# Kernel optimization log

Measured on AMD Instinct MI355X. Metric: run time of the kernel, lower is better.

## Reference

```python
import jax, jax.numpy as jnp
import numpy as np

D_MODEL = 1024
N_HEADS = 16
DEPTH = D_MODEL // N_HEADS
B, S = 2, 2048


def setup_inputs() -> dict:
    key = jax.random.key(0)
    ks = jax.random.split(key, 11)
    scale = 1.0 / np.sqrt(D_MODEL)
    return {
        "q": jax.random.normal(ks[0], (B, S, D_MODEL), jnp.float32),
        "k": jax.random.normal(ks[1], (B, S, D_MODEL), jnp.float32),
        "v": jax.random.normal(ks[2], (B, S, D_MODEL), jnp.float32),
        "wq": jax.random.normal(ks[3], (D_MODEL, D_MODEL), jnp.float32) * scale,
        "bq": jnp.zeros((D_MODEL,), jnp.float32),
        "wk": jax.random.normal(ks[4], (D_MODEL, D_MODEL), jnp.float32) * scale,
        "bk": jnp.zeros((D_MODEL,), jnp.float32),
        "wv": jax.random.normal(ks[5], (D_MODEL, D_MODEL), jnp.float32) * scale,
        "bv": jnp.zeros((D_MODEL,), jnp.float32),
        "wo": jax.random.normal(ks[6], (D_MODEL, D_MODEL), jnp.float32) * scale,
        "bo": jnp.zeros((D_MODEL,), jnp.float32),
    }


def _mha(q, k, v, wq, bq, wk, bk, wv, bv, wo, bo):
    b, s, _ = q.shape
    # separate QKV projections
    qh = (q @ wq + bq).reshape(b, s, N_HEADS, DEPTH).transpose(0, 2, 1, 3)  # [b,h,s,d]
    kh = (k @ wk + bk).reshape(b, s, N_HEADS, DEPTH).transpose(0, 2, 1, 3)
    vh = (v @ wv + bv).reshape(b, s, N_HEADS, DEPTH).transpose(0, 2, 1, 3)
    # keras.layers.Attention default: UNSCALED dot-product scores, causal mask
    scores = jnp.einsum("bhqd,bhkd->bhqk", qh, kh)  # [b,h,s,s]
    causal = jnp.tril(jnp.ones((s, s), bool))
    scores = jnp.where(causal, scores, jnp.float32(-1e9))
    attn = jax.nn.softmax(scores, axis=-1)
    out = jnp.einsum("bhqk,bhkd->bhqd", attn, vh)  # [b,h,s,d]
    out = out.transpose(0, 2, 1, 3).reshape(b, s, D_MODEL)
    return out @ wo + bo


def reference(q, k, v, wq, bq, wk, bk, wv, bv, wo, bo):
    return _mha(q, k, v, wq, bq, wk, bk, wv, bv, wo, bo)
```

## Files before the change

### kernel.cpp

```cpp
#include <hip/hip_runtime.h>
#include <stdint.h>

#define AS1q __attribute__((address_space(1)))
#define AS3q __attribute__((address_space(3)))

typedef unsigned short US;
typedef __bf16 bf16x8 __attribute__((ext_vector_type(8)));
typedef float f32x4 __attribute__((ext_vector_type(4)));
typedef float f32x16 __attribute__((ext_vector_type(16)));
typedef float f32x2 __attribute__((ext_vector_type(2)));
typedef __bf16 bf16x2 __attribute__((ext_vector_type(2)));

#define LOG2E 1.44269504088896340736f

__device__ __forceinline__ US f2bf(float f) {
  union { float f; uint32_t u; } c; c.f = f;
  uint32_t u = c.u;
  return (US)((u + 0x7fffu + ((u >> 16) & 1u)) >> 16);
}

__device__ __forceinline__ bf16x8 asb(uint4 u) {
  union { uint4 u; bf16x8 b; } c; c.u = u; return c.b;
}

__device__ __forceinline__ uint32_t pk2(float a, float b) {
  f32x2 fv; fv[0] = a; fv[1] = b;
  bf16x2 bb = __builtin_convertvector(fv, bf16x2);
  union { bf16x2 b; uint32_t u; } c; c.b = bb; return c.u;
}

__device__ __forceinline__ void gload16(const void* g, void* l) {
  __builtin_amdgcn_global_load_lds((AS1q void*)(void*)g, (AS3q void*)l, 16, 0, 0);
}

__global__ void prep_kernel(const float* __restrict__ q, const float* __restrict__ k,
                            const float* __restrict__ v,
                            const float* __restrict__ w0, const float* __restrict__ w1,
                            const float* __restrict__ w2, const float* __restrict__ w3,
                            US* __restrict__ qb, US* __restrict__ kb, US* __restrict__ vb,
                            US* __restrict__ t0, US* __restrict__ t1,
                            US* __restrict__ t2, US* __restrict__ t3) {
  __shared__ US T[64 * 68];
  const int bx = blockIdx.x;
  const int t = threadIdx.x;
  if (bx < 6144) {
    const int ten = bx >> 11, chunk = bx & 2047;
    const float* s; US* d;
    if (ten == 0)      { s = q; d = qb; }
    else if (ten == 1) { s = k; d = kb; }
    else               { s = v; d = vb; }
    int i = (chunk * 256 + t) * 8;
    float4 f0 = *(const float4*)&s[i];
    float4 f1 = *(const float4*)&s[i + 4];
    ushort4 u0, u1;
    u0.x = f2bf(f0.x); u0.y = f2bf(f0.y); u0.z = f2bf(f0.z); u0.w = f2bf(f0.w);
    u1.x = f2bf(f1.x); u1.y = f2bf(f1.y); u1.z = f2bf(f1.z); u1.w = f2bf(f1.w);
    *(ushort4*)&d[i] = u0;
    *(ushort4*)&d[i + 4] = u1;
    return;
  }
  const int idx = bx - 6144;
  const int wsel = idx >> 8, rem = idx & 255;
  const int n0 = (rem & 15) * 64, k0 = (rem >> 4) * 64;
  const float* W; US* Wt;
  if (wsel == 0)      { W = w0; Wt = t0; }
  else if (wsel == 1) { W = w1; Wt = t1; }
  else if (wsel == 2) { W = w2; Wt = t2; }
  else                { W = w3; Wt = t3; }
#pragma unroll
  for (int it = 0; it < 4; ++it) {
    int p = t + it * 256;
    int row = p >> 4, c4 = (p & 15) * 4;
    float4 f = *(const float4*)&W[(k0 + row) * 1024 + n0 + c4];
    ushort4 u;
    u.x = f2bf(f.x); u.y = f2bf(f.y); u.z = f2bf(f.z); u.w = f2bf(f.w);
    *(ushort4*)&T[row * 68 + c4] = u;
  }
  __syncthreads();
#pragma unroll
  for (int it = 0; it < 4; ++it) {
    int p = t + it * 256;
    int rn = p >> 4, ck = (p & 15) * 4;
    ushort4 o;
    o.x = T[(ck + 0) * 68 + rn];
    o.y = T[(ck + 1) * 68 + rn];
    o.z = T[(ck + 2) * 68 + rn];
    o.w = T[(ck + 3) * 68 + rn];
    *(ushort4*)&Wt[(n0 + rn) * 1024 + k0 + ck] = o;
  }
}

template <bool SWAP>
__device__ __forceinline__ void gemm_core(const US* A, const US* Wt,
                                          int m0, int n0, US* As, US* Bs,
                                          f32x4 acc[4][4]) {
  const int tid = threadIdx.x;
  const int wave = tid >> 6, lane = tid & 63;
  const int quad = lane >> 4, l16 = lane & 15;
  const int wm = wave >> 1, wn = wave & 1;
#pragma unroll
  for (int i = 0; i < 4; ++i)
#pragma unroll
    for (int j = 0; j < 4; ++j) acc[i][j] = (f32x4)0.0f;
  const int p = wave * 64 + lane;
  const int arow0 = p >> 2, koff = (p & 3) * 8;
  for (int k0 = 0; k0 < 1024; k0 += 32) {
    gload16(A + (m0 + arow0) * 1024 + k0 + koff, As + wave * 512);
    gload16(A + (m0 + arow0 + 64) * 1024 + k0 + koff, As + 2048 + wave * 512);
    gload16(Wt + (n0 + arow0) * 1024 + k0 + koff, Bs + wave * 512);
    gload16(Wt + (n0 + arow0 + 64) * 1024 + k0 + koff, Bs + 2048 + wave * 512);
    __syncthreads();
    uint4 af[4], bf_[4];
#pragma unroll
    for (int mt = 0; mt < 4; ++mt)
      af[mt] = *(const uint4*)&As[(wm * 64 + mt * 16 + l16) * 32 + quad * 8];
#pragma unroll
    for (int nt = 0; nt < 4; ++nt)
      bf_[nt] = *(const uint4*)&Bs[(wn * 64 + nt * 16 + l16) * 32 + quad * 8];
#pragma unroll
    for (int i = 0; i < 4; ++i)
#pragma unroll
      for (int j = 0; j < 4; ++j) {
        if (SWAP)
          acc[i][j] = __builtin_amdgcn_mfma_f32_16x16x32_bf16(asb(bf_[i]), asb(af[j]),
                                                              acc[i][j], 0, 0, 0);
        else
          acc[i][j] = __builtin_amdgcn_mfma_f32_16x16x32_bf16(asb(af[i]), asb(bf_[j]),
                                                              acc[i][j], 0, 0, 0);
      }
    __syncthreads();
  }
}

__global__ __launch_bounds__(256, 4) void gemm_qkv_kernel(
    const US* __restrict__ qb, const US* __restrict__ kb, const US* __restrict__ vb,
    const US* __restrict__ wfT,
    const float* __restrict__ bq, const float* __restrict__ bk, const float* __restrict__ bv,
    US* __restrict__ qh, US* __restrict__ kh, US* __restrict__ vt) {
  __shared__ __align__(16) US As[4096], Bs[4096];
  const int m0 = blockIdx.x * 128, n0 = blockIdx.y * 128;
  const int which = n0 >> 10;
  const int nl0 = n0 & 1023;
  const US* A = (which == 0) ? qb : (which == 1) ? kb : vb;
  const float* bias = (which == 0) ? bq : (which == 1) ? bk : bv;
  const int tid = threadIdx.x, wave = tid >> 6, lane = tid & 63;
  const int quad = lane >> 4, l16 = lane & 15;
  const int wm = wave >> 1, wn = wave & 1;
  f32x4 acc[4][4];
  if (which == 2) {
    gemm_core<true>(A, wfT, m0, n0, As, Bs, acc);
#pragma unroll
    for (int nt = 0; nt < 4; ++nt) {
      int dg = nl0 + wn * 64 + nt * 16 + quad * 4;
#pragma unroll
      for (int r = 0; r < 4; ++r) {
        int d = dg + r;
        float bval = bias[d];
        int hh = d >> 6, dd = d & 63;
#pragma unroll
        for (int mt = 0; mt < 4; ++mt) {
          int sg = m0 + wm * 64 + mt * 16;
          int bb = sg >> 11, ss = sg & 2047;
          vt[(((size_t)bb * 16 + hh) * 64 + dd) * 2048 + ss + l16] =
              f2bf(acc[nt][mt][r] + bval);
        }
      }
    }
  } else {
    gemm_core<false>(A, wfT, m0, n0, As, Bs, acc);
    US* O = (which == 0) ? qh : kh;
    const float scale = (which == 0) ? LOG2E : 1.0f;
#pragma unroll
    for (int nt = 0; nt < 4; ++nt) {
      int nl = nl0 + wn * 64 + nt * 16 + l16;
      float bval = bias[nl];
      int hh = nl >> 6, d = nl & 63;
#pragma unroll
      for (int mt = 0; mt < 4; ++mt) {
#pragma unroll
        for (int r = 0; r < 4; ++r) {
          int m = m0 + wm * 64 + mt * 16 + quad * 4 + r;
          int bb = m >> 11, s = m & 2047;
          O[((bb * 16 + hh) * 2048 + s) * 64 + d] = f2bf((acc[mt][nt][r] + bval) * scale);
        }
      }
    }
  }
}

__global__ __launch_bounds__(256, 4) void gemm_out_kernel(
    const US* __restrict__ ao, const US* __restrict__ woT,
    const float* __restrict__ bo, float* __restrict__ out) {
  __shared__ __align__(16) US As[4096], Bs[2048];
  const int m0 = blockIdx.x * 128, n0 = blockIdx.y * 64;
  const int tid = threadIdx.x;
  const int wave = tid >> 6, lane = tid & 63;
  const int quad = lane >> 4, l16 = lane & 15;
  f32x4 acc[2][4];
#pragma unroll
  for (int i = 0; i < 2; ++i)
#pragma unroll
    for (int j = 0; j < 4; ++j) acc[i][j] = (f32x4)0.0f;
  const int arow0 = tid >> 2, koff = (tid & 3) * 8;
  for (int k0 = 0; k0 < 1024; k0 += 32) {
    gload16(ao + (m0 + arow0) * 1024 + k0 + koff, As + wave * 512);
    gload16(ao + (m0 + arow0 + 64) * 1024 + k0 + koff, As + 2048 + wave * 512);
    gload16(woT + (n0 + arow0) * 1024 + k0 + koff, Bs + wave * 512);
    __syncthreads();
    uint4 af[2], bf_[4];
#pragma unroll
    for (int mt = 0; mt < 2; ++mt)
      af[mt] = *(const uint4*)&As[(wave * 32 + mt * 16 + l16) * 32 + quad * 8];
#pragma unroll
    for (int nt = 0; nt < 4; ++nt)
      bf_[nt] = *(const uint4*)&Bs[(nt * 16 + l16) * 32 + quad * 8];
#pragma unroll
    for (int mt = 0; mt < 2; ++mt)
#pragma unroll
      for (int nt = 0; nt < 4; ++nt)
        acc[mt][nt] = __builtin_amdgcn_mfma_f32_16x16x32_bf16(asb(af[mt]), asb(bf_[nt]),
                                                              acc[mt][nt], 0, 0, 0);
    __syncthreads();
  }
#pragma unroll
  for (int nt = 0; nt < 4; ++nt) {
    int n = n0 + nt * 16 + l16;
    float bval = bo[n];
#pragma unroll
    for (int mt = 0; mt < 2; ++mt) {
#pragma unroll
      for (int r = 0; r < 4; ++r) {
        int m = m0 + wave * 32 + mt * 16 + quad * 4 + r;
        out[m * 1024 + n] = acc[mt][nt][r] + bval;
      }
    }
  }
}

__global__ __launch_bounds__(512, 4) void attn_kernel(
    const US* __restrict__ qh, const US* __restrict__ kh,
    const US* __restrict__ vt, US* __restrict__ aout) {
  __shared__ __align__(16) char arena[73728];
  US* KsA = (US*)arena;
  US* VsA = (US*)(arena + 32768);
  US* Qs  = (US*)(arena + 65536);
  float* Oex = (float*)arena;
  float* lEx = (float*)(arena + 69632);

  const int tid = threadIdx.x;
  const int wave = tid >> 6, lane = tid & 63;
  const int l31 = lane & 31, lh = lane >> 5;
  const int w_m = wave & 1, w_k = wave >> 1;
  const int bh = blockIdx.x;
  const int b = bh >> 4, h = bh & 15;
  const int jg = blockIdx.y;

  const US* gkb = kh + (size_t)bh * 2048 * 64;
  const US* gvb = vt + (size_t)bh * 64 * 2048;

  for (int ei = 0; ei < 2; ++ei) {
    const int qt = ei ? jg : (31 - jg);
    const int q0 = qt * 64;
    const int nit = (qt >> 1) + 1;
    __syncthreads();
    {
      const US* gq = qh + ((size_t)bh * 2048 + q0) * 64;
      {
        int p = tid;
        int row = p >> 3, c = (p & 7) ^ (row & 7);
        gload16(gq + row * 64 + c * 8, Qs + wave * 512);
      }
#pragma unroll
      for (int ro = 0; ro < 2; ++ro) {
        int p = tid + ro * 512;
        int row = p >> 3, c = (p & 7) ^ (row & 7);
        gload16(gkb + row * 64 + c * 8, KsA + ro * 4096 + wave * 512);
      }
#pragma unroll
      for (int ro = 0; ro < 2; ++ro) {
        int p = tid + ro * 512;
        int row = p >> 4, c = (p & 15) ^ (row & 15);
        gload16(gvb + row * 2048 + c * 8, VsA + ro * 4096 + wave * 512);
      }
    }
    __syncthreads();

    const int qrow = w_m * 32 + l31;
    uint4 bq[4];
#pragma unroll
    for (int s = 0; s < 4; ++s)
      bq[s] = *(const uint4*)&Qs[qrow * 64 + (((2 * s + lh) ^ (qrow & 7)) * 8)];
    const int q_g = q0 + qrow;

    float l_lane = 0.0f;
    f32x16 Oa0 = (f32x16)0.0f, Oa1 = (f32x16)0.0f;

    for (int it = 0; it < nit; ++it) {
      const int cb = it & 1;
      const int kb = it * 128;
      if (it) __syncthreads();
      if (it + 1 < nit) {
        const US* gk = gkb + (kb + 128) * 64;
        const US* gv = gvb + (kb + 128);
        US* kd = KsA + (cb ^ 1) * 8192;
        US* vd = VsA + (cb ^ 1) * 8192;
#pragma unroll
        for (int ro = 0; ro < 2; ++ro) {
          int p = tid + ro * 512;
          int row = p >> 3, c = (p & 7) ^ (row & 7);
          gload16(gk + row * 64 + c * 8, kd + ro * 4096 + wave * 512);
        }
#pragma unroll
        for (int ro = 0; ro < 2; ++ro) {
          int p = tid + ro * 512;
          int row = p >> 4, c = (p & 15) ^ (row & 15);
          gload16(gv + row * 2048 + c * 8, vd + ro * 4096 + wave * 512);
        }
      }
      const US* Kc = KsA + cb * 8192;
      const US* Vc = VsA + cb * 8192;

      f32x16 sa0 = (f32x16)0.0f;
      const int kr0 = w_k * 32 + l31;
#pragma unroll
      for (int s = 0; s < 4; ++s) {
        uint4 ka0 = *(const uint4*)&Kc[kr0 * 64 + (((2 * s + lh) ^ (kr0 & 7)) * 8)];
        sa0 = __builtin_amdgcn_mfma_f32_32x32x16_bf16(asb(ka0), asb(bq[s]), sa0, 0, 0, 0);
      }

      const bool diag = (it == nit - 1);
      float e[16];
      const int kbase = kb + w_k * 32 + 4 * lh;
#pragma unroll
      for (int r = 0; r < 16; ++r) {
        float ev = __builtin_amdgcn_exp2f(sa0[r]);
        if (diag) {
          int key_g = kbase + (r & 3) + 8 * (r >> 2);
          if (key_g > q_g) ev = 0.0f;
        }
        e[r] = ev;
        l_lane += ev;
      }

#pragma unroll
      for (int s2 = 0; s2 < 2; ++s2) {
        uint32_t PA0 = pk2(e[8 * s2 + 0], e[8 * s2 + 1]);
        uint32_t PA1 = pk2(e[8 * s2 + 2], e[8 * s2 + 3]);
        uint32_t PB0 = pk2(e[8 * s2 + 4], e[8 * s2 + 5]);
        uint32_t PB1 = pk2(e[8 * s2 + 6], e[8 * s2 + 7]);
        uint32_t XA0 = (uint32_t)__shfl_xor((int)PA0, 32, 64);
        uint32_t XA1 = (uint32_t)__shfl_xor((int)PA1, 32, 64);
        uint32_t XB0 = (uint32_t)__shfl_xor((int)PB0, 32, 64);
        uint32_t XB1 = (uint32_t)__shfl_xor((int)PB1, 32, 64);
        uint4 bp;
        bp.x = lh ? XB0 : PA0;
        bp.y = lh ? XB1 : PA1;
        bp.z = lh ? PB0 : XA0;
        bp.w = lh ? PB1 : XA1;
        const int c_log = w_k * 4 + s2 * 2 + lh;
        int vr0 = l31;
        uint4 va0 = *(const uint4*)&Vc[vr0 * 128 + ((c_log ^ (vr0 & 15)) * 8)];
        Oa0 = __builtin_amdgcn_mfma_f32_32x32x16_bf16(asb(va0), asb(bp), Oa0, 0, 0, 0);
        int vr1 = 32 + l31;
        uint4 va1 = *(const uint4*)&Vc[vr1 * 128 + ((c_log ^ (vr1 & 15)) * 8)];
        Oa1 = __builtin_amdgcn_mfma_f32_32x32x16_bf16(asb(va1), asb(bp), Oa1, 0, 0, 0);
      }
    }

    float l_q = l_lane + __shfl_xor(l_lane, 32, 64);

    __syncthreads();
    {
      float* myO = Oex + w_k * (64 * 68);
      int q_idx = w_m * 32 + l31;
#pragma unroll
      for (int r = 0; r < 16; ++r) {
        int dr = 4 * lh + (r & 3) + 8 * (r >> 2);
        myO[q_idx * 68 + dr] = Oa0[r];
        myO[q_idx * 68 + 32 + dr] = Oa1[r];
      }
      if (lh == 0) lEx[w_k * 64 + q_idx] = l_q;
    }
    __syncthreads();
    {
      int q_idx = tid >> 3;
      int dseg = (tid & 7) * 8;
      float inv = 1.0f / (lEx[q_idx] + lEx[64 + q_idx] + lEx[128 + q_idx] + lEx[192 + q_idx]);
      union { US s[8]; uint4 v; } ob;
#pragma unroll
      for (int t2 = 0; t2 < 8; ++t2) {
        float o = Oex[q_idx * 68 + dseg + t2]
                + Oex[64 * 68 + q_idx * 68 + dseg + t2]
                + Oex[2 * 64 * 68 + q_idx * 68 + dseg + t2]
                + Oex[3 * 64 * 68 + q_idx * 68 + dseg + t2];
        ob.s[t2] = f2bf(o * inv);
      }
      US* dst = aout + ((size_t)b * 2048 + q0 + q_idx) * 1024 + h * 64 + dseg;
      *(uint4*)dst = ob.v;
    }
  }
}

extern "C" void kernel_launch(void* const* d_in, const int* in_sizes, int n_in,
                              void* d_out, int out_size, void* d_ws, size_t ws_size,
                              hipStream_t stream) {
  const float* q  = (const float*)d_in[0];
  const float* k  = (const float*)d_in[1];
  const float* v  = (const float*)d_in[2];
  const float* wq = (const float*)d_in[3];
  const float* bq = (const float*)d_in[4];
  const float* wk = (const float*)d_in[5];
  const float* bk = (const float*)d_in[6];
  const float* wv = (const float*)d_in[7];
  const float* bv = (const float*)d_in[8];
  const float* wo = (const float*)d_in[9];
  const float* bo = (const float*)d_in[10];
  float* out = (float*)d_out;

  char* ws = (char*)d_ws;
  const size_t MB = 1024 * 1024;
  US* qb  = (US*)(ws + 0 * MB);
  US* kb  = (US*)(ws + 8 * MB);
  US* vb  = (US*)(ws + 16 * MB);
  US* wqT = (US*)(ws + 24 * MB);
  US* wkT = (US*)(ws + 26 * MB);
  US* wvT = (US*)(ws + 28 * MB);
  US* woT = (US*)(ws + 30 * MB);
  US* qh  = (US*)(ws + 32 * MB);
  US* kh  = (US*)(ws + 40 * MB);
  US* vt  = (US*)(ws + 48 * MB);
  US* ao  = (US*)(ws + 56 * MB);

  prep_kernel<<<7168, 256, 0, stream>>>(q, k, v, wq, wk, wv, wo,
                                        qb, kb, vb, wqT, wkT, wvT, woT);
  gemm_qkv_kernel<<<dim3(32, 24), 256, 0, stream>>>(qb, kb, vb, wqT,
                                                    bq, bk, bv, qh, kh, vt);
  attn_kernel<<<dim3(32, 16), 512, 0, stream>>>(qh, kh, vt, ao);
  gemm_out_kernel<<<dim3(32, 16), 256, 0, stream>>>(ao, woT, bo, out);
}
```

Before: 205.7 us.

## Rewrite QKV GEMM as 256x256 tiles with double-buffered swizzled LDS pipeline

The QKV projection GEMM moves from 128x128 tiles with a 32-wide K step and a sync per step to 256x256 tiles with 512 threads. It uses a 64-wide K step, an XOR-swizzled LDS layout and double buffering, with async global-to-LDS loads interleaved between MFMA phases and explicit vmcnt waits and barriers. The goal is to hide load latency, cut LDS bank conflicts and raise data reuse per block. In exchange it uses 128KB of LDS and launches only 192 blocks, which may underfill the GPU, and the attention kernel's launch bounds are relaxed to 2 blocks per CU.

```diff
diff --git a/kernel.cpp b/kernel.cpp
--- a/kernel.cpp
+++ b/kernel.cpp
@@ -32,6 +32,14 @@
 __device__ __forceinline__ void gload16(const void* g, void* l) {
   __builtin_amdgcn_global_load_lds((AS1q void*)(void*)g, (AS3q void*)l, 16, 0, 0);
 }
+
+__device__ __forceinline__ void bar() {
+  asm volatile("" ::: "memory");
+  __builtin_amdgcn_s_barrier();
+  asm volatile("" ::: "memory");
+}
+
+#define VM8 asm volatile("s_waitcnt vmcnt(8)" ::: "memory")
 
 __global__ void prep_kernel(const float* __restrict__ q, const float* __restrict__ k,
                             const float* __restrict__ v,
@@ -90,98 +98,161 @@
   }
 }
 
+#define STA(t, P) gload16(gA + (size_t)(P) * 65536 + (t) * 64, lA + ((t) & 1) * 16384 + (P) * 4096)
+#define STB(t, P) gload16(gB + (size_t)(P) * 65536 + (t) * 64, lB + ((t) & 1) * 16384 + (P) * 4096)
+
+#define MM(d, a, b) d = __builtin_amdgcn_mfma_f32_16x16x32_bf16(asb(a), asb(b), d, 0, 0, 0)
+
+#define PHASE(MF0, STAGE_CODE, VMW)                                                      \
+  {                                                                                      \
+    uint4 ar0[2], ar1[2];                                                                \
+    {                                                                                    \
+      const int row0 = arowb + (MF0) * 16;                                               \
+      const int row1 = arowb + (MF0) * 16 + 16;                                          \
+      ar0[0] = *(const uint4*)&Ab[row0 * 64 + (((0 + quad) ^ (row0 & 7)) << 3)];         \
+      ar0[1] = *(const uint4*)&Ab[row0 * 64 + (((4 + quad) ^ (row0 & 7)) << 3)];         \
+      ar1[0] = *(const uint4*)&Ab[row1 * 64 + (((0 + quad) ^ (row1 & 7)) << 3)];         \
+      ar1[1] = *(const uint4*)&Ab[row1 * 64 + (((4 + quad) ^ (row1 & 7)) << 3)];         \
+    }                                                                                    \
+    STAGE_CODE;                                                                          \
+    bar();                                                                               \
+    __builtin_amdgcn_s_setprio(1);                                                       \
+    _Pragma("unroll") for (int nf = 0; nf < 4; ++nf) {                                   \
+      if constexpr (SWAP) {                                                              \
+        MM(acc[MF0][nf], br[nf][0], ar0[0]);                                             \
+        MM(acc[MF0][nf], br[nf][1], ar0[1]);                                             \
+        MM(acc[(MF0) + 1][nf], br[nf][0], ar1[0]);                                       \
+        MM(acc[(MF0) + 1][nf], br[nf][1], ar1[1]);                                       \
+      } else {                                                                           \
+        MM(acc[MF0][nf], ar0[0], br[nf][0]);                                             \
+        MM(acc[MF0][nf], ar0[1], br[nf][1]);                                             \
+        MM(acc[(MF0) + 1][nf], ar1[0], br[nf][0]);                                       \
+        MM(acc[(MF0) + 1][nf], ar1[1], br[nf][1]);                                       \
+      }                                                                                  \
+    }                                                                                    \
+    __builtin_amdgcn_s_setprio(0);                                                       \
+    VMW;                                                                                 \
+    bar();                                                                               \
+  }
+
 template <bool SWAP>
-__device__ __forceinline__ void gemm_core(const US* A, const US* Wt,
-                                          int m0, int n0, US* As, US* Bs,
-                                          f32x4 acc[4][4]) {
+__device__ __forceinline__ void qkv8_core(const US* __restrict__ A, const US* __restrict__ Bw,
+                                          int m0, US* Al, US* Bl, f32x4 acc[8][4]) {
   const int tid = threadIdx.x;
   const int wave = tid >> 6, lane = tid & 63;
   const int quad = lane >> 4, l16 = lane & 15;
-  const int wm = wave >> 1, wn = wave & 1;
-#pragma unroll
-  for (int i = 0; i < 4; ++i)
+  const int wm2 = wave >> 2, wn4 = wave & 3;
+#pragma unroll
+  for (int i = 0; i < 8; ++i)
 #pragma unroll
     for (int j = 0; j < 4; ++j) acc[i][j] = (f32x4)0.0f;
-  const int p = wave * 64 + lane;
-  const int arow0 = p >> 2, koff = (p & 3) * 8;
-  for (int k0 = 0; k0 < 1024; k0 += 32) {
-    gload16(A + (m0 + arow0) * 1024 + k0 + koff, As + wave * 512);
-    gload16(A + (m0 + arow0 + 64) * 1024 + k0 + koff, As + 2048 + wave * 512);
-    gload16(Wt + (n0 + arow0) * 1024 + k0 + koff, Bs + wave * 512);
-    gload16(Wt + (n0 + arow0 + 64) * 1024 + k0 + koff, Bs + 2048 + wave * 512);
-    __syncthreads();
-    uint4 af[4], bf_[4];
-#pragma unroll
-    for (int mt = 0; mt < 4; ++mt)
-      af[mt] = *(const uint4*)&As[(wm * 64 + mt * 16 + l16) * 32 + quad * 8];
-#pragma unroll
-    for (int nt = 0; nt < 4; ++nt)
-      bf_[nt] = *(const uint4*)&Bs[(wn * 64 + nt * 16 + l16) * 32 + quad * 8];
-#pragma unroll
-    for (int i = 0; i < 4; ++i)
-#pragma unroll
-      for (int j = 0; j < 4; ++j) {
-        if (SWAP)
-          acc[i][j] = __builtin_amdgcn_mfma_f32_16x16x32_bf16(asb(bf_[i]), asb(af[j]),
-                                                              acc[i][j], 0, 0, 0);
-        else
-          acc[i][j] = __builtin_amdgcn_mfma_f32_16x16x32_bf16(asb(af[i]), asb(bf_[j]),
-                                                              acc[i][j], 0, 0, 0);
-      }
-    __syncthreads();
-  }
-}
-
-__global__ __launch_bounds__(256, 4) void gemm_qkv_kernel(
+
+  const int srow = tid >> 3;
+  const int sch = (tid & 7) ^ (srow & 7);
+  const US* gA = A + (size_t)(m0 + srow) * 1024 + sch * 8;
+  const US* gB = Bw + (size_t)srow * 1024 + sch * 8;
+  US* lA = Al + wave * 512;
+  US* lB = Bl + wave * 512;
+
+  STA(0, 0); STA(0, 1); STA(0, 2); STA(0, 3);
+  STB(0, 0); STB(0, 1); STB(0, 2); STB(0, 3);
+  STB(1, 0); STB(1, 1); STB(1, 2); STB(1, 3);
+  STA(1, 0); STA(1, 2);
+  asm volatile("s_waitcnt vmcnt(6)" ::: "memory");
+  bar();
+
+  const int arowb = wm2 * 128 + l16;
+  const int browb = wn4 * 64 + l16;
+
+  for (int i = 0; i < 8; ++i) {
+    const int ti1 = 2 * i + 1, ti2 = 2 * i + 2, ti3 = 2 * i + 3;
+    const bool more = (i < 7);
+    {
+      const US* Ab = Al;
+      const US* Bb = Bl;
+      uint4 br[4][2];
+#pragma unroll
+      for (int nf = 0; nf < 4; ++nf) {
+        const int row = browb + nf * 16;
+        br[nf][0] = *(const uint4*)&Bb[row * 64 + (((0 + quad) ^ (row & 7)) << 3)];
+        br[nf][1] = *(const uint4*)&Bb[row * 64 + (((4 + quad) ^ (row & 7)) << 3)];
+      }
+      PHASE(0, { STA(ti1, 1); STA(ti1, 3); }, )
+      PHASE(2, { if (more) { STB(ti2, 0); STB(ti2, 1); } }, VM8)
+      PHASE(4, { if (more) { STA(ti2, 0); STA(ti2, 2); } }, )
+      PHASE(6, { if (more) { STB(ti2, 2); STB(ti2, 3); } }, VM8)
+    }
+    {
+      const US* Ab = Al + 16384;
+      const US* Bb = Bl + 16384;
+      uint4 br[4][2];
+#pragma unroll
+      for (int nf = 0; nf < 4; ++nf) {
+        const int row = browb + nf * 16;
+        br[nf][0] = *(const uint4*)&Bb[row * 64 + (((0 + quad) ^ (row & 7)) << 3)];
+        br[nf][1] = *(const uint4*)&Bb[row * 64 + (((4 + quad) ^ (row & 7)) << 3)];
+      }
+      PHASE(0, { if (more) { STA(ti2, 1); STA(ti2, 3); } }, )
+      PHASE(2, { if (more) { STB(ti3, 0); STB(ti3, 1); } }, VM8)
+      PHASE(4, { if (more) { STA(ti3, 0); STA(ti3, 2); } }, )
+      PHASE(6, { if (more) { STB(ti3, 2); STB(ti3, 3); } }, VM8)
+    }
+  }
+}
+
+__global__ __launch_bounds__(512, 2) void gemm_qkv_kernel(
     const US* __restrict__ qb, const US* __restrict__ kb, const US* __restrict__ vb,
     const US* __restrict__ wfT,
     const float* __restrict__ bq, const float* __restrict__ bk, const float* __restrict__ bv,
     US* __restrict__ qh, US* __restrict__ kh, US* __restrict__ vt) {
-  __shared__ __align__(16) US As[4096], Bs[4096];
-  const int m0 = blockIdx.x * 128, n0 = blockIdx.y * 128;
-  const int which = n0 >> 10;
-  const int nl0 = n0 & 1023;
+  __shared__ __align__(16) US Al[2 * 16384], Bl[2 * 16384];
+  const int m0 = blockIdx.x * 256;
+  const int nb = blockIdx.y;
+  const int which = nb >> 2;
+  const int n0loc = (nb & 3) * 256;
   const US* A = (which == 0) ? qb : (which == 1) ? kb : vb;
   const float* bias = (which == 0) ? bq : (which == 1) ? bk : bv;
-  const int tid = threadIdx.x, wave = tid >> 6, lane = tid & 63;
+  const US* Bw = wfT + ((size_t)which * 1024 + n0loc) * 1024;
+
+  const int tid = threadIdx.x;
+  const int wave = tid >> 6, lane = tid & 63;
   const int quad = lane >> 4, l16 = lane & 15;
-  const int wm = wave >> 1, wn = wave & 1;
-  f32x4 acc[4][4];
+  const int wm2 = wave >> 2, wn4 = wave & 3;
+
+  f32x4 acc[8][4];
   if (which == 2) {
-    gemm_core<true>(A, wfT, m0, n0, As, Bs, acc);
-#pragma unroll
-    for (int nt = 0; nt < 4; ++nt) {
-      int dg = nl0 + wn * 64 + nt * 16 + quad * 4;
+    qkv8_core<true>(A, Bw, m0, Al, Bl, acc);
+#pragma unroll
+    for (int nf = 0; nf < 4; ++nf) {
 #pragma unroll
       for (int r = 0; r < 4; ++r) {
-        int d = dg + r;
-        float bval = bias[d];
-        int hh = d >> 6, dd = d & 63;
-#pragma unroll
-        for (int mt = 0; mt < 4; ++mt) {
-          int sg = m0 + wm * 64 + mt * 16;
-          int bb = sg >> 11, ss = sg & 2047;
-          vt[(((size_t)bb * 16 + hh) * 64 + dd) * 2048 + ss + l16] =
-              f2bf(acc[nt][mt][r] + bval);
+        const int dg = n0loc + wn4 * 64 + nf * 16 + quad * 4 + r;
+        const float bval = bias[dg];
+        const int hh = dg >> 6, dd = dg & 63;
+#pragma unroll
+        for (int mf = 0; mf < 8; ++mf) {
+          const int m = m0 + wm2 * 128 + mf * 16 + l16;
+          const int bb = m >> 11, ss = m & 2047;
+          vt[(((size_t)bb * 16 + hh) * 64 + dd) * 2048 + ss] = f2bf(acc[mf][nf][r] + bval);
         }
       }
     }
   } else {
-    gemm_core<false>(A, wfT, m0, n0, As, Bs, acc);
+    qkv8_core<false>(A, Bw, m0, Al, Bl, acc);
     US* O = (which == 0) ? qh : kh;
     const float scale = (which == 0) ? LOG2E : 1.0f;
 #pragma unroll
-    for (int nt = 0; nt < 4; ++nt) {
-      int nl = nl0 + wn * 64 + nt * 16 + l16;
-      float bval = bias[nl];
-      int hh = nl >> 6, d = nl & 63;
-#pragma unroll
-      for (int mt = 0; mt < 4; ++mt) {
+    for (int nf = 0; nf < 4; ++nf) {
+      const int nl = n0loc + wn4 * 64 + nf * 16 + l16;
+      const float bval = bias[nl];
+      const int hh = nl >> 6, d = nl & 63;
+#pragma unroll
+      for (int mf = 0; mf < 8; ++mf) {
 #pragma unroll
         for (int r = 0; r < 4; ++r) {
-          int m = m0 + wm * 64 + mt * 16 + quad * 4 + r;
-          int bb = m >> 11, s = m & 2047;
-          O[((bb * 16 + hh) * 2048 + s) * 64 + d] = f2bf((acc[mt][nt][r] + bval) * scale);
+          const int m = m0 + wm2 * 128 + mf * 16 + quad * 4 + r;
+          const int bb = m >> 11, ss = m & 2047;
+          O[(((size_t)bb * 16 + hh) * 2048 + ss) * 64 + d] = f2bf((acc[mf][nf][r] + bval) * scale);
         }
       }
     }
@@ -237,7 +308,7 @@
   }
 }
 
-__global__ __launch_bounds__(512, 4) void attn_kernel(
+__global__ __launch_bounds__(512, 2) void attn_kernel(
     const US* __restrict__ qh, const US* __restrict__ kh,
     const US* __restrict__ vt, US* __restrict__ aout) {
   __shared__ __align__(16) char arena[73728];
@@ -433,7 +504,7 @@
 
   prep_kernel<<<7168, 256, 0, stream>>>(q, k, v, wq, wk, wv, wo,
                                         qb, kb, vb, wqT, wkT, wvT, woT);
-  gemm_qkv_kernel<<<dim3(32, 24), 256, 0, stream>>>(qb, kb, vb, wqT,
+  gemm_qkv_kernel<<<dim3(16, 12), 512, 0, stream>>>(qb, kb, vb, wqT,
                                                     bq, bk, bv, qh, kh, vt);
   attn_kernel<<<dim3(32, 16), 512, 0, stream>>>(qh, kh, vt, ao);
   gemm_out_kernel<<<dim3(32, 16), 256, 0, stream>>>(ao, woT, bo, out);
```

Result: slower. 212.4 us (+3.3%).

## Widen GEMM K-step to 64 with XOR-swizzled LDS, halve attention shuffles

Applied to the files above, without the earlier changes.

Both projection GEMMs now stage 64-wide K tiles per iteration with an XOR-swizzled shared-memory layout. This halves the number of barrier pairs and is meant to avoid LDS bank conflicts on fragment reads, at the cost of doubled shared memory per block. The attention kernel's P-matrix lane exchange now uses two shuffles instead of four, selecting which half to send based on lane half. Its launch bounds drop from 4 to 2 minimum blocks, which relaxes the register cap.

```diff
diff --git a/kernel.cpp b/kernel.cpp
--- a/kernel.cpp
+++ b/kernel.cpp
@@ -91,9 +91,9 @@
 }
 
 template <bool SWAP>
-__device__ __forceinline__ void gemm_core(const US* A, const US* Wt,
-                                          int m0, int n0, US* As, US* Bs,
-                                          f32x4 acc[4][4]) {
+__device__ __forceinline__ void gemm_core64(const US* A, const US* Wt,
+                                            int m0, int n0, US* As, US* Bs,
+                                            f32x4 acc[4][4]) {
   const int tid = threadIdx.x;
   const int wave = tid >> 6, lane = tid & 63;
   const int quad = lane >> 4, l16 = lane & 15;
@@ -102,31 +102,49 @@
   for (int i = 0; i < 4; ++i)
 #pragma unroll
     for (int j = 0; j < 4; ++j) acc[i][j] = (f32x4)0.0f;
-  const int p = wave * 64 + lane;
-  const int arow0 = p >> 2, koff = (p & 3) * 8;
-  for (int k0 = 0; k0 < 1024; k0 += 32) {
-    gload16(A + (m0 + arow0) * 1024 + k0 + koff, As + wave * 512);
-    gload16(A + (m0 + arow0 + 64) * 1024 + k0 + koff, As + 2048 + wave * 512);
-    gload16(Wt + (n0 + arow0) * 1024 + k0 + koff, Bs + wave * 512);
-    gload16(Wt + (n0 + arow0 + 64) * 1024 + k0 + koff, Bs + 2048 + wave * 512);
-    __syncthreads();
-    uint4 af[4], bf_[4];
-#pragma unroll
-    for (int mt = 0; mt < 4; ++mt)
-      af[mt] = *(const uint4*)&As[(wm * 64 + mt * 16 + l16) * 32 + quad * 8];
-#pragma unroll
-    for (int nt = 0; nt < 4; ++nt)
-      bf_[nt] = *(const uint4*)&Bs[(wn * 64 + nt * 16 + l16) * 32 + quad * 8];
+
+  const int srow = tid >> 3;
+  const int sch = (tid & 7) ^ (srow & 7);
+  const US* gA = A + (size_t)(m0 + srow) * 1024 + sch * 8;
+  const US* gB = Wt + (size_t)(n0 + srow) * 1024 + sch * 8;
+  US* lA = As + wave * 512;
+  US* lB = Bs + wave * 512;
+
+  for (int k0 = 0; k0 < 1024; k0 += 64) {
+#pragma unroll
+    for (int c = 0; c < 4; ++c) {
+      gload16(gA + (size_t)c * 32 * 1024 + k0, lA + c * 2048);
+      gload16(gB + (size_t)c * 32 * 1024 + k0, lB + c * 2048);
+    }
+    __syncthreads();
+    uint4 af[4][2], bf_[4][2];
+#pragma unroll
+    for (int mt = 0; mt < 4; ++mt) {
+      const int row = wm * 64 + mt * 16 + l16;
+      af[mt][0] = *(const uint4*)&As[row * 64 + ((quad ^ (row & 7)) << 3)];
+      af[mt][1] = *(const uint4*)&As[row * 64 + (((4 + quad) ^ (row & 7)) << 3)];
+    }
+#pragma unroll
+    for (int nt = 0; nt < 4; ++nt) {
+      const int row = wn * 64 + nt * 16 + l16;
+      bf_[nt][0] = *(const uint4*)&Bs[row * 64 + ((quad ^ (row & 7)) << 3)];
+      bf_[nt][1] = *(const uint4*)&Bs[row * 64 + (((4 + quad) ^ (row & 7)) << 3)];
+    }
 #pragma unroll
     for (int i = 0; i < 4; ++i)
 #pragma unroll
       for (int j = 0; j < 4; ++j) {
-        if (SWAP)
-          acc[i][j] = __builtin_amdgcn_mfma_f32_16x16x32_bf16(asb(bf_[i]), asb(af[j]),
+        if (SWAP) {
+          acc[i][j] = __builtin_amdgcn_mfma_f32_16x16x32_bf16(asb(bf_[i][0]), asb(af[j][0]),
                                                               acc[i][j], 0, 0, 0);
-        else
-          acc[i][j] = __builtin_amdgcn_mfma_f32_16x16x32_bf16(asb(af[i]), asb(bf_[j]),
+          acc[i][j] = __builtin_amdgcn_mfma_f32_16x16x32_bf16(asb(bf_[i][1]), asb(af[j][1]),
                                                               acc[i][j], 0, 0, 0);
+        } else {
+          acc[i][j] = __builtin_amdgcn_mfma_f32_16x16x32_bf16(asb(af[i][0]), asb(bf_[j][0]),
+                                                              acc[i][j], 0, 0, 0);
+          acc[i][j] = __builtin_amdgcn_mfma_f32_16x16x32_bf16(asb(af[i][1]), asb(bf_[j][1]),
+                                                              acc[i][j], 0, 0, 0);
+        }
       }
     __syncthreads();
   }
@@ -137,7 +155,7 @@
     const US* __restrict__ wfT,
     const float* __restrict__ bq, const float* __restrict__ bk, const float* __restrict__ bv,
     US* __restrict__ qh, US* __restrict__ kh, US* __restrict__ vt) {
-  __shared__ __align__(16) US As[4096], Bs[4096];
+  __shared__ __align__(16) US As[8192], Bs[8192];
   const int m0 = blockIdx.x * 128, n0 = blockIdx.y * 128;
   const int which = n0 >> 10;
   const int nl0 = n0 & 1023;
@@ -148,7 +166,7 @@
   const int wm = wave >> 1, wn = wave & 1;
   f32x4 acc[4][4];
   if (which == 2) {
-    gemm_core<true>(A, wfT, m0, n0, As, Bs, acc);
+    gemm_core64<true>(A, wfT, m0, n0, As, Bs, acc);
 #pragma unroll
     for (int nt = 0; nt < 4; ++nt) {
       int dg = nl0 + wn * 64 + nt * 16 + quad * 4;
@@ -167,7 +185,7 @@
       }
     }
   } else {
-    gemm_core<false>(A, wfT, m0, n0, As, Bs, acc);
+    gemm_core64<false>(A, wfT, m0, n0, As, Bs, acc);
     US* O = (which == 0) ? qh : kh;
     const float scale = (which == 0) ? LOG2E : 1.0f;
 #pragma unroll
@@ -191,7 +209,7 @@
 __global__ __launch_bounds__(256, 4) void gemm_out_kernel(
     const US* __restrict__ ao, const US* __restrict__ woT,
     const float* __restrict__ bo, float* __restrict__ out) {
-  __shared__ __align__(16) US As[4096], Bs[2048];
+  __shared__ __align__(16) US As[8192], Bs[4096];
   const int m0 = blockIdx.x * 128, n0 = blockIdx.y * 64;
   const int tid = threadIdx.x;
   const int wave = tid >> 6, lane = tid & 63;
@@ -201,25 +219,44 @@
   for (int i = 0; i < 2; ++i)
 #pragma unroll
     for (int j = 0; j < 4; ++j) acc[i][j] = (f32x4)0.0f;
-  const int arow0 = tid >> 2, koff = (tid & 3) * 8;
-  for (int k0 = 0; k0 < 1024; k0 += 32) {
-    gload16(ao + (m0 + arow0) * 1024 + k0 + koff, As + wave * 512);
-    gload16(ao + (m0 + arow0 + 64) * 1024 + k0 + koff, As + 2048 + wave * 512);
-    gload16(woT + (n0 + arow0) * 1024 + k0 + koff, Bs + wave * 512);
-    __syncthreads();
-    uint4 af[2], bf_[4];
+
+  const int srow = tid >> 3;
+  const int sch = (tid & 7) ^ (srow & 7);
+  const US* gA = ao + (size_t)(m0 + srow) * 1024 + sch * 8;
+  const US* gB = woT + (size_t)(n0 + srow) * 1024 + sch * 8;
+  US* lA = As + wave * 512;
+  US* lB = Bs + wave * 512;
+
+  for (int k0 = 0; k0 < 1024; k0 += 64) {
+#pragma unroll
+    for (int c = 0; c < 4; ++c)
+      gload16(gA + (size_t)c * 32 * 1024 + k0, lA + c * 2048);
+#pragma unroll
+    for (int c = 0; c < 2; ++c)
+      gload16(gB + (size_t)c * 32 * 1024 + k0, lB + c * 2048);
+    __syncthreads();
+    uint4 af[2][2], bf_[4][2];
+#pragma unroll
+    for (int mt = 0; mt < 2; ++mt) {
+      const int row = wave * 32 + mt * 16 + l16;
+      af[mt][0] = *(const uint4*)&As[row * 64 + ((quad ^ (row & 7)) << 3)];
+      af[mt][1] = *(const uint4*)&As[row * 64 + (((4 + quad) ^ (row & 7)) << 3)];
+    }
+#pragma unroll
+    for (int nt = 0; nt < 4; ++nt) {
+      const int row = nt * 16 + l16;
+      bf_[nt][0] = *(const uint4*)&Bs[row * 64 + ((quad ^ (row & 7)) << 3)];
+      bf_[nt][1] = *(const uint4*)&Bs[row * 64 + (((4 + quad) ^ (row & 7)) << 3)];
+    }
 #pragma unroll
     for (int mt = 0; mt < 2; ++mt)
-      af[mt] = *(const uint4*)&As[(wave * 32 + mt * 16 + l16) * 32 + quad * 8];
-#pragma unroll
-    for (int nt = 0; nt < 4; ++nt)
-      bf_[nt] = *(const uint4*)&Bs[(nt * 16 + l16) * 32 + quad * 8];
-#pragma unroll
-    for (int mt = 0; mt < 2; ++mt)
-#pragma unroll
-      for (int nt = 0; nt < 4; ++nt)
-        acc[mt][nt] = __builtin_amdgcn_mfma_f32_16x16x32_bf16(asb(af[mt]), asb(bf_[nt]),
+#pragma unroll
+      for (int nt = 0; nt < 4; ++nt) {
+        acc[mt][nt] = __builtin_amdgcn_mfma_f32_16x16x32_bf16(asb(af[mt][0]), asb(bf_[nt][0]),
                                                               acc[mt][nt], 0, 0, 0);
+        acc[mt][nt] = __builtin_amdgcn_mfma_f32_16x16x32_bf16(asb(af[mt][1]), asb(bf_[nt][1]),
+                                                              acc[mt][nt], 0, 0, 0);
+      }
     __syncthreads();
   }
 #pragma unroll
@@ -237,7 +274,7 @@
   }
 }
 
-__global__ __launch_bounds__(512, 4) void attn_kernel(
+__global__ __launch_bounds__(512, 2) void attn_kernel(
     const US* __restrict__ qh, const US* __restrict__ kh,
     const US* __restrict__ vt, US* __restrict__ aout) {
   __shared__ __align__(16) char arena[73728];
@@ -348,15 +385,13 @@
         uint32_t PA1 = pk2(e[8 * s2 + 2], e[8 * s2 + 3]);
         uint32_t PB0 = pk2(e[8 * s2 + 4], e[8 * s2 + 5]);
         uint32_t PB1 = pk2(e[8 * s2 + 6], e[8 * s2 + 7]);
-        uint32_t XA0 = (uint32_t)__shfl_xor((int)PA0, 32, 64);
-        uint32_t XA1 = (uint32_t)__shfl_xor((int)PA1, 32, 64);
-        uint32_t XB0 = (uint32_t)__shfl_xor((int)PB0, 32, 64);
-        uint32_t XB1 = (uint32_t)__shfl_xor((int)PB1, 32, 64);
+        uint32_t W0 = (uint32_t)__shfl_xor((int)(lh ? PA0 : PB0), 32, 64);
+        uint32_t W1 = (uint32_t)__shfl_xor((int)(lh ? PA1 : PB1), 32, 64);
         uint4 bp;
-        bp.x = lh ? XB0 : PA0;
-        bp.y = lh ? XB1 : PA1;
-        bp.z = lh ? PB0 : XA0;
-        bp.w = lh ? PB1 : XA1;
+        bp.x = lh ? W0 : PA0;
+        bp.y = lh ? W1 : PA1;
+        bp.z = lh ? PB0 : W0;
+        bp.w = lh ? PB1 : W1;
         const int c_log = w_k * 4 + s2 * 2 + lh;
         int vr0 = l31;
         uint4 va0 = *(const uint4*)&Vc[vr0 * 128 + ((c_log ^ (vr0 & 15)) * 8)];
```

After: 199.6 us (median of 3 runs). -3.0%, faster.
